# Kernel tuning notes

Hardware: AMD Instinct MI355X
Metric: run time of the kernel (lower is better)

Reference implementation:

```python
import jax, jax.numpy as jnp
import numpy as np

B, R, C, NH = 8, 64, 256, 8
N = R * R            # 4096 tokens
HD = C // NH         # head dim 32
FF = 3               # focusing factor

def dwconv(x, w, b):
    # x: (B, C, H, W); w: (C, 1, kh, kw) depthwise
    y = jax.lax.conv_general_dilated(
        x, w, window_strides=(1, 1), padding='SAME',
        dimension_numbers=('NCHW', 'OIHW', 'NCHW'),
        feature_group_count=x.shape[1])
    return y + b[None, :, None, None]

def setup_inputs() -> dict:
    key = jax.random.key(0)
    ks = jax.random.split(key, 6)
    return {
        'qkv': jax.random.normal(ks[0], (3, B, N, C), jnp.float32),
        'pos_enc': jax.random.normal(ks[1], (1, N, C), jnp.float32) * 0.02,
        'scale': jax.random.normal(ks[2], (1, 1, C), jnp.float32) * 0.02,
        'w_v': jax.random.normal(ks[3], (C, 1, 3, 3), jnp.float32) * 0.1,
        'b_v': jnp.zeros((C,), jnp.float32),
        'w_dwc': jax.random.normal(ks[4], (HD, 1, 5, 5), jnp.float32) * 0.1,
        'b_dwc': jnp.zeros((HD,), jnp.float32),
    }

def reference(qkv, pos_enc, scale, w_v, b_v, w_dwc, b_dwc):
    q, k, v = qkv[0], qkv[1], qkv[2]          # each (B, N, C)
    # --- LePE: depthwise 3x3 conv on v over full channel dim ---
    v_img = v.transpose(0, 2, 1).reshape(B, C, R, R)
    lepe = dwconv(v_img, w_v, b_v)            # (B, C, R, R)
    lepe = lepe.reshape(B * NH, HD, N).transpose(0, 2, 1)   # (B*h, N, hd)
    v = v_img.reshape(B, C, N).transpose(0, 2, 1)           # (B, N, C)
    # --- focused kernelization ---
    k = k + pos_enc
    sc = jax.nn.softplus(scale)
    q = (jax.nn.relu(q) + 1e-6) / sc
    k = (jax.nn.relu(k) + 1e-6) / sc
    qn = jnp.linalg.norm(q, axis=-1, keepdims=True)
    kn = jnp.linalg.norm(k, axis=-1, keepdims=True)
    q = q ** FF
    k = k ** FF
    q = q / jnp.linalg.norm(q, axis=-1, keepdims=True) * qn
    k = k / jnp.linalg.norm(k, axis=-1, keepdims=True) * kn
    split = lambda x: x.reshape(B, N, NH, HD).transpose(0, 2, 1, 3).reshape(B * NH, N, HD)
    q, k, v = split(q), split(k), split(v)    # (B*h, N, hd)
    # --- linear attention (kv aggregation path: N >> hd) ---
    z = 1.0 / (jnp.einsum('bic,bc->bi', q, k.sum(axis=1)) + 1e-6)
    kv = jnp.einsum('bjc,bjd->bcd', k, v)     # (B*h, hd, hd)
    x = jnp.einsum('bic,bcd,bi->bid', q, kv, z)
    # --- dwc feature mixing on v per head ---
    fm = v.transpose(0, 2, 1).reshape(B * NH, HD, R, R)
    fm = dwconv(fm, w_dwc, b_dwc).reshape(B * NH, HD, N).transpose(0, 2, 1)
    x = x + fm + lepe
    x = x.reshape(B, NH, N, HD).transpose(0, 2, 1, 3).reshape(B, N, C)
    return x
```

## Files before the change

kernel.cpp:

```cpp
#include <hip/hip_runtime.h>
#include <math.h>

#define B_  8
#define R_  64
#define C_  256
#define NH_ 8
#define N_  4096
#define HD_ 32

__device__ __forceinline__ float softplus_rcp(float s) {
    return 1.f / __logf(1.f + __expf(s));
}

__global__ __launch_bounds__(256) void kernelN(
        const float* __restrict__ qkv, const float* __restrict__ pos,
        const float* __restrict__ scale,
        float* __restrict__ qs_arr, float* __restrict__ ks_arr) {
    const int t    = threadIdx.x;
    const int wave = t >> 6, lane = t & 63;
    const int tok  = blockIdx.x * 4 + wave;
    const int n    = tok & (N_ - 1);
    const int c0   = lane * 4;

    const size_t qidx = (size_t)tok * C_ + c0;
    const float4 q4 = *(const float4*)(qkv + qidx);
    const float4 k4 = *(const float4*)(qkv + (size_t)B_ * N_ * C_ + qidx);
    const float4 p4 = *(const float4*)(pos + (size_t)n * C_ + c0);
    const float4 s4 = *(const float4*)(scale + c0);

    float qa[4] = {q4.x, q4.y, q4.z, q4.w};
    float ka[4] = {k4.x, k4.y, k4.z, k4.w};
    float pa[4] = {p4.x, p4.y, p4.z, p4.w};
    float sa[4] = {s4.x, s4.y, s4.z, s4.w};

    float sq2 = 0.f, sq6 = 0.f, sk2 = 0.f, sk6 = 0.f;
    #pragma unroll
    for (int i = 0; i < 4; i++) {
        const float rsc = softplus_rcp(sa[i]);
        const float qv = (fmaxf(qa[i], 0.f) + 1e-6f) * rsc;
        const float kv = (fmaxf(ka[i] + pa[i], 0.f) + 1e-6f) * rsc;
        sq2 += qv * qv;  sk2 += kv * kv;
        const float q3 = qv * qv * qv, k3 = kv * kv * kv;
        sq6 += q3 * q3;  sk6 += k3 * k3;
    }
    #pragma unroll
    for (int m = 1; m < 64; m <<= 1) {
        sq2 += __shfl_xor(sq2, m, 64);
        sq6 += __shfl_xor(sq6, m, 64);
        sk2 += __shfl_xor(sk2, m, 64);
        sk6 += __shfl_xor(sk6, m, 64);
    }
    if (lane == 0) {
        qs_arr[tok] = sqrtf(sq2) * rsqrtf(sq6);
        ks_arr[tok] = sqrtf(sk2) * rsqrtf(sk6);
    }
}

__global__ __launch_bounds__(256) void kernelB2(
        const float* __restrict__ qkv, const float* __restrict__ pos,
        const float* __restrict__ scale, const float* __restrict__ ks_arr,
        float* __restrict__ kv_ws, float* __restrict__ ksum_ws) {
    __shared__ float k_s[128 * HD_];
    __shared__ float v_s[128 * HD_];
    __shared__ float rsc_s[HD_];
    const int t     = threadIdx.x;
    const int bh    = blockIdx.x >> 3;
    const int chunk = blockIdx.x & 7;
    const int b     = bh >> 3, h = bh & 7;
    const int c     = t >> 3, p = t & 7, dbase = p * 4;

    if (t < HD_) rsc_s[t] = softplus_rcp(scale[h * HD_ + t]);
    __syncthreads();

    float a0 = 0.f, a1 = 0.f, a2 = 0.f, a3 = 0.f, ksp = 0.f;
    const size_t kbase = (size_t)B_ * N_ * C_ + (size_t)b * N_ * C_ + h * HD_;
    const size_t vbase = (size_t)2 * B_ * N_ * C_ + (size_t)b * N_ * C_ + h * HD_;
    const int tokbase = b * N_;

    for (int tile = 0; tile < 4; tile++) {
        const int n0 = chunk * 512 + tile * 128;
        #pragma unroll
        for (int i = 0; i < 4; i++) {
            const int j  = (i * 256 + t) * 4;
            const int nl = j >> 5, d = j & 31;
            const float4 kr = *(const float4*)(qkv + kbase + (size_t)(n0 + nl) * C_ + d);
            const float4 pr = *(const float4*)(pos + (size_t)(n0 + nl) * C_ + h * HD_ + d);
            const float ksn = ks_arr[tokbase + n0 + nl];
            float4 o;
            {
                float v0 = (fmaxf(kr.x + pr.x, 0.f) + 1e-6f) * rsc_s[d + 0];
                float v1 = (fmaxf(kr.y + pr.y, 0.f) + 1e-6f) * rsc_s[d + 1];
                float v2 = (fmaxf(kr.z + pr.z, 0.f) + 1e-6f) * rsc_s[d + 2];
                float v3 = (fmaxf(kr.w + pr.w, 0.f) + 1e-6f) * rsc_s[d + 3];
                o.x = v0 * v0 * v0 * ksn;  o.y = v1 * v1 * v1 * ksn;
                o.z = v2 * v2 * v2 * ksn;  o.w = v3 * v3 * v3 * ksn;
            }
            *(float4*)&k_s[j] = o;
            ((float4*)v_s)[i * 256 + t] =
                *(const float4*)(qkv + vbase + (size_t)(n0 + nl) * C_ + d);
        }
        __syncthreads();
        #pragma unroll 4
        for (int nl = 0; nl < 128; nl++) {
            const float  kc = k_s[nl * HD_ + c];
            const float4 vv = *(const float4*)&v_s[nl * HD_ + dbase];
            a0 = fmaf(kc, vv.x, a0);
            a1 = fmaf(kc, vv.y, a1);
            a2 = fmaf(kc, vv.z, a2);
            a3 = fmaf(kc, vv.w, a3);
        }
        #pragma unroll
        for (int i = 0; i < 16; i++)
            ksp += k_s[(p + i * 8) * HD_ + c];
        __syncthreads();
    }
    float* kvdst = kv_ws + (size_t)bh * 1024 + c * HD_ + dbase;
    atomicAdd(kvdst + 0, a0);
    atomicAdd(kvdst + 1, a1);
    atomicAdd(kvdst + 2, a2);
    atomicAdd(kvdst + 3, a3);
    k_s[c * 8 + p] = ksp;
    __syncthreads();
    if (t < 32) {
        float s = 0.f;
        #pragma unroll
        for (int i = 0; i < 8; i++) s += k_s[t * 8 + i];
        atomicAdd(&ksum_ws[bh * HD_ + t], s);
    }
}

__global__ __launch_bounds__(256) void kernelCD2(
        const float* __restrict__ qkv, const float* __restrict__ qs_arr,
        const float* __restrict__ kv_ws, const float* __restrict__ ksum_ws,
        const float* __restrict__ scale,
        const float* __restrict__ w_v,  const float* __restrict__ b_v,
        const float* __restrict__ w_dwc, const float* __restrict__ b_dwc,
        float* __restrict__ out) {
    __shared__ float v_s[20 * 20 * 32];
    __shared__ float kv_s[1024];
    __shared__ float ks_s[32];
    __shared__ float rsc_s[32];
    const int t    = threadIdx.x;
    const int tile = blockIdx.x;
    const int h    = blockIdx.y;
    const int b    = blockIdx.z;
    const int ty0  = (tile >> 2) * 16, tx0 = (tile & 3) * 16;
    const int bh   = b * NH_ + h;

    ((float4*)kv_s)[t] = ((const float4*)(kv_ws + (size_t)bh * 1024))[t];
    if (t < 32) {
        ks_s[t]  = ksum_ws[bh * HD_ + t];
        rsc_s[t] = softplus_rcp(scale[h * HD_ + t]);
    }

    const float* vb = qkv + (size_t)2 * B_ * N_ * C_ + (size_t)b * N_ * C_ + h * HD_;
    #pragma unroll
    for (int i = 0; i < 13; i++) {
        const int idx = i * 256 + t;
        if (idx < 3200) {
            const int pix = idx >> 3, d4 = (idx & 7) * 4;
            const int yy = pix / 20, xx = pix - yy * 20;
            const int gy = ty0 + yy - 2, gx = tx0 + xx - 2;
            float4 val = make_float4(0.f, 0.f, 0.f, 0.f);
            if (gy >= 0 && gy < R_ && gx >= 0 && gx < R_)
                val = *(const float4*)(vb + (size_t)(gy * R_ + gx) * C_ + d4);
            *(float4*)&v_s[pix * 32 + d4] = val;
        }
    }

    const int c  = t & 31, pg = t >> 5;
    float wv[9], wd[25];
    {
        const float* wvp = w_v + (size_t)(h * HD_ + c) * 9;
        const float* wdp = w_dwc + (size_t)c * 25;
        #pragma unroll
        for (int i = 0; i < 9; i++)  wv[i] = wvp[i];
        #pragma unroll
        for (int i = 0; i < 25; i++) wd[i] = wdp[i];
    }
    const float bias = b_v[h * HD_ + c] + b_dwc[c];
    __syncthreads();

    float res[32];
    #pragma unroll
    for (int r2 = 0; r2 < 2; r2++) {
        const int ty = pg * 2 + r2;
        float win[5][5];
        #pragma unroll
        for (int j = 0; j < 5; j++)
            #pragma unroll
            for (int i = 0; i < 5; i++)
                win[j][i] = v_s[((ty + i) * 20 + j) * 32 + c];
        #pragma unroll
        for (int tx = 0; tx < 16; tx++) {
            float a = bias;
            #pragma unroll
            for (int j = 0; j < 5; j++) {
                const int slot = (tx + j) % 5;
                #pragma unroll
                for (int i = 0; i < 5; i++)
                    a = fmaf(wd[i * 5 + j], win[slot][i], a);
            }
            #pragma unroll
            for (int j = 1; j < 4; j++) {
                const int slot = (tx + j) % 5;
                #pragma unroll
                for (int i = 1; i < 4; i++)
                    a = fmaf(wv[(i - 1) * 3 + (j - 1)], win[slot][i], a);
            }
            res[r2 * 16 + tx] = a;
            if (tx < 15) {
                const int slot = tx % 5;
                #pragma unroll
                for (int i = 0; i < 5; i++)
                    win[slot][i] = v_s[((ty + i) * 20 + (tx + 5)) * 32 + c];
            }
        }
    }
    __syncthreads();
    #pragma unroll
    for (int r2 = 0; r2 < 2; r2++)
        #pragma unroll
        for (int tx = 0; tx < 16; tx++)
            v_s[((pg * 2 + r2) * 16 + tx) * 33 + c] = res[r2 * 16 + tx];
    __syncthreads();

    {
        const int tyy = t >> 4, txx = t & 15;
        const int n   = (ty0 + tyy) * R_ + (tx0 + txx);
        const int tok = b * N_ + n;
        float q[32];
        const float4* qsrc = (const float4*)(qkv + (size_t)tok * C_ + h * HD_);
        #pragma unroll
        for (int i = 0; i < 8; i++) ((float4*)q)[i] = qsrc[i];
        const float qs = qs_arr[tok];
        #pragma unroll
        for (int i = 0; i < 32; i++) {
            const float r = (fmaxf(q[i], 0.f) + 1e-6f) * rsc_s[i];
            q[i] = r * r * r * qs;
        }

        float denom = 1e-6f;
        #pragma unroll
        for (int cc = 0; cc < 32; cc++) denom = fmaf(q[cc], ks_s[cc], denom);
        const float z = 1.f / denom;

        float o[32];
        #pragma unroll
        for (int i = 0; i < 32; i++) o[i] = 0.f;
        #pragma unroll
        for (int cc = 0; cc < 32; cc++) {
            const float qc = q[cc];
            #pragma unroll
            for (int d = 0; d < 32; d++)
                o[d] = fmaf(qc, kv_s[cc * 32 + d], o[d]);
        }
        float4* dst = (float4*)(out + (size_t)tok * C_ + h * HD_);
        #pragma unroll
        for (int i = 0; i < 8; i++) {
            float4 v4;
            v4.x = fmaf(o[i*4+0], z, v_s[t * 33 + i*4+0]);
            v4.y = fmaf(o[i*4+1], z, v_s[t * 33 + i*4+1]);
            v4.z = fmaf(o[i*4+2], z, v_s[t * 33 + i*4+2]);
            v4.w = fmaf(o[i*4+3], z, v_s[t * 33 + i*4+3]);
            dst[i] = v4;
        }
    }
}

extern "C" void kernel_launch(void* const* d_in, const int* in_sizes, int n_in,
                              void* d_out, int out_size, void* d_ws, size_t ws_size,
                              hipStream_t stream) {
    const float* qkv   = (const float*)d_in[0];
    const float* pos   = (const float*)d_in[1];
    const float* scale = (const float*)d_in[2];
    const float* w_v   = (const float*)d_in[3];
    const float* b_v   = (const float*)d_in[4];
    const float* w_dwc = (const float*)d_in[5];
    const float* b_dwc = (const float*)d_in[6];
    float* out = (float*)d_out;

    float* qs_arr  = (float*)d_ws;
    float* ks_arr  = qs_arr + (size_t)B_ * N_;
    float* kv_ws   = ks_arr + (size_t)B_ * N_;
    float* ksum_ws = kv_ws + 64 * 1024;

    (void)hipMemsetAsync(kv_ws, 0, (64 * 1024 + 64 * 32) * sizeof(float), stream);
    kernelN<<<dim3(B_ * N_ / 4), 256, 0, stream>>>(qkv, pos, scale, qs_arr, ks_arr);
    kernelB2<<<dim3(512), 256, 0, stream>>>(qkv, pos, scale, ks_arr, kv_ws, ksum_ws);
    kernelCD2<<<dim3(16, NH_, B_), 256, 0, stream>>>(qkv, qs_arr, kv_ws, ksum_ws,
                                                     scale, w_v, b_v, w_dwc, b_dwc, out);
}
```

Before: 222.8 us.

## Store conv tile and result exchange in bf16 LDS; double kv-reduction grid

The fused conv/attention kernel now keeps the v halo tile and the conv results in LDS as bf16 instead of fp32, which roughly halves its LDS footprint and should allow more resident blocks. Conv results are written straight into a separate padded exchange buffer, so the register array and one barrier are gone. The kv-aggregation kernel's grid is doubled, with each block covering half as many tokens. The cost is bf16 rounding on v and on the conv outputs, which lowers accuracy, and twice as many atomic adds into the kv workspace.

```diff
diff --git a/kernel.cpp b/kernel.cpp
--- a/kernel.cpp
+++ b/kernel.cpp
@@ -10,6 +10,14 @@
 
 __device__ __forceinline__ float softplus_rcp(float s) {
     return 1.f / __logf(1.f + __expf(s));
+}
+__device__ __forceinline__ unsigned short f2bf(float f) {
+    unsigned u = __float_as_uint(f);
+    u += 0x7FFFu + ((u >> 16) & 1u);
+    return (unsigned short)(u >> 16);
+}
+__device__ __forceinline__ float bf2f(unsigned short h) {
+    return __uint_as_float(((unsigned)h) << 16);
 }
 
 __global__ __launch_bounds__(256) void kernelN(
@@ -64,8 +72,8 @@
     __shared__ float v_s[128 * HD_];
     __shared__ float rsc_s[HD_];
     const int t     = threadIdx.x;
-    const int bh    = blockIdx.x >> 3;
-    const int chunk = blockIdx.x & 7;
+    const int bh    = blockIdx.x >> 4;
+    const int chunk = blockIdx.x & 15;
     const int b     = bh >> 3, h = bh & 7;
     const int c     = t >> 3, p = t & 7, dbase = p * 4;
 
@@ -77,8 +85,8 @@
     const size_t vbase = (size_t)2 * B_ * N_ * C_ + (size_t)b * N_ * C_ + h * HD_;
     const int tokbase = b * N_;
 
-    for (int tile = 0; tile < 4; tile++) {
-        const int n0 = chunk * 512 + tile * 128;
+    for (int tile = 0; tile < 2; tile++) {
+        const int n0 = chunk * 256 + tile * 128;
         #pragma unroll
         for (int i = 0; i < 4; i++) {
             const int j  = (i * 256 + t) * 4;
@@ -129,14 +137,16 @@
     }
 }
 
-__global__ __launch_bounds__(256) void kernelCD2(
+#define EXP_ 258
+__global__ __launch_bounds__(256) void kernelCD3(
         const float* __restrict__ qkv, const float* __restrict__ qs_arr,
         const float* __restrict__ kv_ws, const float* __restrict__ ksum_ws,
         const float* __restrict__ scale,
         const float* __restrict__ w_v,  const float* __restrict__ b_v,
         const float* __restrict__ w_dwc, const float* __restrict__ b_dwc,
         float* __restrict__ out) {
-    __shared__ float v_s[20 * 20 * 32];
+    __shared__ unsigned short v_s[20 * 20 * 32];
+    __shared__ unsigned short exch[HD_ * EXP_];
     __shared__ float kv_s[1024];
     __shared__ float ks_s[32];
     __shared__ float rsc_s[32];
@@ -164,7 +174,10 @@
             float4 val = make_float4(0.f, 0.f, 0.f, 0.f);
             if (gy >= 0 && gy < R_ && gx >= 0 && gx < R_)
                 val = *(const float4*)(vb + (size_t)(gy * R_ + gx) * C_ + d4);
-            *(float4*)&v_s[pix * 32 + d4] = val;
+            ushort4 hv;
+            hv.x = f2bf(val.x);  hv.y = f2bf(val.y);
+            hv.z = f2bf(val.z);  hv.w = f2bf(val.w);
+            *(ushort4*)&v_s[pix * 32 + d4] = hv;
         }
     }
 
@@ -181,7 +194,6 @@
     const float bias = b_v[h * HD_ + c] + b_dwc[c];
     __syncthreads();
 
-    float res[32];
     #pragma unroll
     for (int r2 = 0; r2 < 2; r2++) {
         const int ty = pg * 2 + r2;
@@ -190,7 +202,7 @@
         for (int j = 0; j < 5; j++)
             #pragma unroll
             for (int i = 0; i < 5; i++)
-                win[j][i] = v_s[((ty + i) * 20 + j) * 32 + c];
+                win[j][i] = bf2f(v_s[((ty + i) * 20 + j) * 32 + c]);
         #pragma unroll
         for (int tx = 0; tx < 16; tx++) {
             float a = bias;
@@ -208,21 +220,15 @@
                 for (int i = 1; i < 4; i++)
                     a = fmaf(wv[(i - 1) * 3 + (j - 1)], win[slot][i], a);
             }
-            res[r2 * 16 + tx] = a;
+            exch[c * EXP_ + (ty * 16 + tx)] = f2bf(a);
             if (tx < 15) {
                 const int slot = tx % 5;
                 #pragma unroll
                 for (int i = 0; i < 5; i++)
-                    win[slot][i] = v_s[((ty + i) * 20 + (tx + 5)) * 32 + c];
-            }
-        }
-    }
-    __syncthreads();
-    #pragma unroll
-    for (int r2 = 0; r2 < 2; r2++)
-        #pragma unroll
-        for (int tx = 0; tx < 16; tx++)
-            v_s[((pg * 2 + r2) * 16 + tx) * 33 + c] = res[r2 * 16 + tx];
+                    win[slot][i] = bf2f(v_s[((ty + i) * 20 + (tx + 5)) * 32 + c]);
+            }
+        }
+    }
     __syncthreads();
 
     {
@@ -259,10 +265,10 @@
         #pragma unroll
         for (int i = 0; i < 8; i++) {
             float4 v4;
-            v4.x = fmaf(o[i*4+0], z, v_s[t * 33 + i*4+0]);
-            v4.y = fmaf(o[i*4+1], z, v_s[t * 33 + i*4+1]);
-            v4.z = fmaf(o[i*4+2], z, v_s[t * 33 + i*4+2]);
-            v4.w = fmaf(o[i*4+3], z, v_s[t * 33 + i*4+3]);
+            v4.x = fmaf(o[i*4+0], z, bf2f(exch[(i*4+0) * EXP_ + t]));
+            v4.y = fmaf(o[i*4+1], z, bf2f(exch[(i*4+1) * EXP_ + t]));
+            v4.z = fmaf(o[i*4+2], z, bf2f(exch[(i*4+2) * EXP_ + t]));
+            v4.w = fmaf(o[i*4+3], z, bf2f(exch[(i*4+3) * EXP_ + t]));
             dst[i] = v4;
         }
     }
@@ -287,7 +293,7 @@
 
     (void)hipMemsetAsync(kv_ws, 0, (64 * 1024 + 64 * 32) * sizeof(float), stream);
     kernelN<<<dim3(B_ * N_ / 4), 256, 0, stream>>>(qkv, pos, scale, qs_arr, ks_arr);
-    kernelB2<<<dim3(512), 256, 0, stream>>>(qkv, pos, scale, ks_arr, kv_ws, ksum_ws);
-    kernelCD2<<<dim3(16, NH_, B_), 256, 0, stream>>>(qkv, qs_arr, kv_ws, ksum_ws,
+    kernelB2<<<dim3(1024), 256, 0, stream>>>(qkv, pos, scale, ks_arr, kv_ws, ksum_ws);
+    kernelCD3<<<dim3(16, NH_, B_), 256, 0, stream>>>(qkv, qs_arr, kv_ws, ksum_ws,
                                                      scale, w_v, b_v, w_dwc, b_dwc, out);
 }
```

Result: no change. 225.5 us (+1.2%).

## Fuse norm computation kernel into KV aggregation kernel

Applied to the files above, without the earlier changes.

Merges the per-token norm kernel into the KV-aggregation kernel. Each block now processes 64 tokens of one batch across all 8 heads, computing q/k norms in-register via 16-lane shuffles. It then forms the per-head KV outer product with a 32-wide per-thread accumulator. This avoids one launch, a second read of k and pos from global memory, and the ks_arr round trip. In exchange it adds many more atomics (32 per thread across 512 blocks) and higher register pressure from acc[32].

```diff
diff --git a/kernel.cpp b/kernel.cpp
--- a/kernel.cpp
+++ b/kernel.cpp
@@ -7,126 +7,111 @@
 #define NH_ 8
 #define N_  4096
 #define HD_ 32
+#define TT_ 16
+#define LDP_ 260
 
 __device__ __forceinline__ float softplus_rcp(float s) {
     return 1.f / __logf(1.f + __expf(s));
 }
 
-__global__ __launch_bounds__(256) void kernelN(
+__global__ __launch_bounds__(256) void kernelNB(
         const float* __restrict__ qkv, const float* __restrict__ pos,
         const float* __restrict__ scale,
-        float* __restrict__ qs_arr, float* __restrict__ ks_arr) {
-    const int t    = threadIdx.x;
-    const int wave = t >> 6, lane = t & 63;
-    const int tok  = blockIdx.x * 4 + wave;
-    const int n    = tok & (N_ - 1);
-    const int c0   = lane * 4;
-
-    const size_t qidx = (size_t)tok * C_ + c0;
-    const float4 q4 = *(const float4*)(qkv + qidx);
-    const float4 k4 = *(const float4*)(qkv + (size_t)B_ * N_ * C_ + qidx);
-    const float4 p4 = *(const float4*)(pos + (size_t)n * C_ + c0);
-    const float4 s4 = *(const float4*)(scale + c0);
-
-    float qa[4] = {q4.x, q4.y, q4.z, q4.w};
-    float ka[4] = {k4.x, k4.y, k4.z, k4.w};
-    float pa[4] = {p4.x, p4.y, p4.z, p4.w};
-    float sa[4] = {s4.x, s4.y, s4.z, s4.w};
-
-    float sq2 = 0.f, sq6 = 0.f, sk2 = 0.f, sk6 = 0.f;
-    #pragma unroll
-    for (int i = 0; i < 4; i++) {
-        const float rsc = softplus_rcp(sa[i]);
-        const float qv = (fmaxf(qa[i], 0.f) + 1e-6f) * rsc;
-        const float kv = (fmaxf(ka[i] + pa[i], 0.f) + 1e-6f) * rsc;
-        sq2 += qv * qv;  sk2 += kv * kv;
-        const float q3 = qv * qv * qv, k3 = kv * kv * kv;
-        sq6 += q3 * q3;  sk6 += k3 * k3;
-    }
-    #pragma unroll
-    for (int m = 1; m < 64; m <<= 1) {
-        sq2 += __shfl_xor(sq2, m, 64);
-        sq6 += __shfl_xor(sq6, m, 64);
-        sk2 += __shfl_xor(sk2, m, 64);
-        sk6 += __shfl_xor(sk6, m, 64);
-    }
-    if (lane == 0) {
-        qs_arr[tok] = sqrtf(sq2) * rsqrtf(sq6);
-        ks_arr[tok] = sqrtf(sk2) * rsqrtf(sk6);
-    }
-}
-
-__global__ __launch_bounds__(256) void kernelB2(
-        const float* __restrict__ qkv, const float* __restrict__ pos,
-        const float* __restrict__ scale, const float* __restrict__ ks_arr,
+        float* __restrict__ qs_arr,
         float* __restrict__ kv_ws, float* __restrict__ ksum_ws) {
-    __shared__ float k_s[128 * HD_];
-    __shared__ float v_s[128 * HD_];
-    __shared__ float rsc_s[HD_];
+    __shared__ float k_s[TT_][LDP_];
+    __shared__ float v_s[TT_][LDP_];
+    __shared__ float rsc_s[C_];
     const int t     = threadIdx.x;
-    const int bh    = blockIdx.x >> 3;
-    const int chunk = blockIdx.x & 7;
-    const int b     = bh >> 3, h = bh & 7;
-    const int c     = t >> 3, p = t & 7, dbase = p * 4;
-
-    if (t < HD_) rsc_s[t] = softplus_rcp(scale[h * HD_ + t]);
-    __syncthreads();
-
-    float a0 = 0.f, a1 = 0.f, a2 = 0.f, a3 = 0.f, ksp = 0.f;
-    const size_t kbase = (size_t)B_ * N_ * C_ + (size_t)b * N_ * C_ + h * HD_;
-    const size_t vbase = (size_t)2 * B_ * N_ * C_ + (size_t)b * N_ * C_ + h * HD_;
-    const int tokbase = b * N_;
+    const int b     = blockIdx.x >> 6;
+    const int chunk = blockIdx.x & 63;
+    const int h  = t >> 5, cc = t & 31;
+    const int tk = t >> 4, sub = t & 15;
+
+    rsc_s[t] = softplus_rcp(scale[t]);
+    __syncthreads();
+
+    float acc[32];
+    #pragma unroll
+    for (int i = 0; i < 32; i++) acc[i] = 0.f;
+    float ksp = 0.f;
+
+    const size_t qbase = (size_t)b * N_ * C_;
+    const size_t kbase = (size_t)(B_ + b) * N_ * C_;
+    const size_t vbase = (size_t)(2 * B_ + b) * N_ * C_;
 
     for (int tile = 0; tile < 4; tile++) {
-        const int n0 = chunk * 512 + tile * 128;
+        const int n0  = chunk * 64 + tile * TT_;
+        const int tok = n0 + tk;
+
+        float kva[16];
+        float sq2 = 0.f, sq6 = 0.f, sk2 = 0.f, sk6 = 0.f;
         #pragma unroll
         for (int i = 0; i < 4; i++) {
-            const int j  = (i * 256 + t) * 4;
-            const int nl = j >> 5, d = j & 31;
-            const float4 kr = *(const float4*)(qkv + kbase + (size_t)(n0 + nl) * C_ + d);
-            const float4 pr = *(const float4*)(pos + (size_t)(n0 + nl) * C_ + h * HD_ + d);
-            const float ksn = ks_arr[tokbase + n0 + nl];
+            const int c0 = (sub + i * 16) * 4;
+            const float4 q4 = *(const float4*)(qkv + qbase + (size_t)tok * C_ + c0);
+            const float4 k4 = *(const float4*)(qkv + kbase + (size_t)tok * C_ + c0);
+            const float4 p4 = *(const float4*)(pos + (size_t)tok * C_ + c0);
+            const float qa[4] = {q4.x, q4.y, q4.z, q4.w};
+            const float ka[4] = {k4.x, k4.y, k4.z, k4.w};
+            const float pa[4] = {p4.x, p4.y, p4.z, p4.w};
+            #pragma unroll
+            for (int j = 0; j < 4; j++) {
+                const float rsc = rsc_s[c0 + j];
+                const float qv = (fmaxf(qa[j], 0.f) + 1e-6f) * rsc;
+                const float kv = (fmaxf(ka[j] + pa[j], 0.f) + 1e-6f) * rsc;
+                sq2 += qv * qv;
+                const float q3 = qv * qv * qv;
+                sq6 += q3 * q3;
+                sk2 += kv * kv;
+                const float k3 = kv * kv * kv;
+                sk6 += k3 * k3;
+                kva[i * 4 + j] = kv;
+            }
+        }
+        #pragma unroll
+        for (int m = 1; m < 16; m <<= 1) {
+            sq2 += __shfl_xor(sq2, m, 64);
+            sq6 += __shfl_xor(sq6, m, 64);
+            sk2 += __shfl_xor(sk2, m, 64);
+            sk6 += __shfl_xor(sk6, m, 64);
+        }
+        const float ksn = sqrtf(sk2) * rsqrtf(sk6);
+        if (sub == 0)
+            qs_arr[b * N_ + tok] = sqrtf(sq2) * rsqrtf(sq6);
+
+        #pragma unroll
+        for (int i = 0; i < 4; i++) {
+            const int c0 = (sub + i * 16) * 4;
             float4 o;
-            {
-                float v0 = (fmaxf(kr.x + pr.x, 0.f) + 1e-6f) * rsc_s[d + 0];
-                float v1 = (fmaxf(kr.y + pr.y, 0.f) + 1e-6f) * rsc_s[d + 1];
-                float v2 = (fmaxf(kr.z + pr.z, 0.f) + 1e-6f) * rsc_s[d + 2];
-                float v3 = (fmaxf(kr.w + pr.w, 0.f) + 1e-6f) * rsc_s[d + 3];
-                o.x = v0 * v0 * v0 * ksn;  o.y = v1 * v1 * v1 * ksn;
-                o.z = v2 * v2 * v2 * ksn;  o.w = v3 * v3 * v3 * ksn;
-            }
-            *(float4*)&k_s[j] = o;
-            ((float4*)v_s)[i * 256 + t] =
-                *(const float4*)(qkv + vbase + (size_t)(n0 + nl) * C_ + d);
+            o.x = kva[i*4+0] * kva[i*4+0] * kva[i*4+0] * ksn;
+            o.y = kva[i*4+1] * kva[i*4+1] * kva[i*4+1] * ksn;
+            o.z = kva[i*4+2] * kva[i*4+2] * kva[i*4+2] * ksn;
+            o.w = kva[i*4+3] * kva[i*4+3] * kva[i*4+3] * ksn;
+            *(float4*)&k_s[tk][c0] = o;
+            *(float4*)&v_s[tk][c0] =
+                *(const float4*)(qkv + vbase + (size_t)tok * C_ + c0);
         }
         __syncthreads();
+
         #pragma unroll 4
-        for (int nl = 0; nl < 128; nl++) {
-            const float  kc = k_s[nl * HD_ + c];
-            const float4 vv = *(const float4*)&v_s[nl * HD_ + dbase];
-            a0 = fmaf(kc, vv.x, a0);
-            a1 = fmaf(kc, vv.y, a1);
-            a2 = fmaf(kc, vv.z, a2);
-            a3 = fmaf(kc, vv.w, a3);
-        }
-        #pragma unroll
-        for (int i = 0; i < 16; i++)
-            ksp += k_s[(p + i * 8) * HD_ + c];
+        for (int nl = 0; nl < TT_; nl++) {
+            const float kc = k_s[nl][h * 32 + cc];
+            ksp += kc;
+            const float* vr = &v_s[nl][h * 32];
+            #pragma unroll
+            for (int d = 0; d < 32; d++)
+                acc[d] = fmaf(kc, vr[d], acc[d]);
+        }
         __syncthreads();
     }
-    float* kvdst = kv_ws + (size_t)bh * 1024 + c * HD_ + dbase;
-    atomicAdd(kvdst + 0, a0);
-    atomicAdd(kvdst + 1, a1);
-    atomicAdd(kvdst + 2, a2);
-    atomicAdd(kvdst + 3, a3);
-    k_s[c * 8 + p] = ksp;
-    __syncthreads();
-    if (t < 32) {
-        float s = 0.f;
-        #pragma unroll
-        for (int i = 0; i < 8; i++) s += k_s[t * 8 + i];
-        atomicAdd(&ksum_ws[bh * HD_ + t], s);
-    }
+
+    const int bh = b * NH_ + h;
+    float* kvdst = kv_ws + (size_t)bh * 1024 + cc * 32;
+    #pragma unroll
+    for (int d = 0; d < 32; d++)
+        atomicAdd(kvdst + d, acc[d]);
+    atomicAdd(&ksum_ws[bh * HD_ + cc], ksp);
 }
 
 __global__ __launch_bounds__(256) void kernelCD2(
@@ -281,13 +266,11 @@
     float* out = (float*)d_out;
 
     float* qs_arr  = (float*)d_ws;
-    float* ks_arr  = qs_arr + (size_t)B_ * N_;
-    float* kv_ws   = ks_arr + (size_t)B_ * N_;
+    float* kv_ws   = qs_arr + (size_t)B_ * N_;
     float* ksum_ws = kv_ws + 64 * 1024;
 
     (void)hipMemsetAsync(kv_ws, 0, (64 * 1024 + 64 * 32) * sizeof(float), stream);
-    kernelN<<<dim3(B_ * N_ / 4), 256, 0, stream>>>(qkv, pos, scale, qs_arr, ks_arr);
-    kernelB2<<<dim3(512), 256, 0, stream>>>(qkv, pos, scale, ks_arr, kv_ws, ksum_ws);
+    kernelNB<<<dim3(512), 256, 0, stream>>>(qkv, pos, scale, qs_arr, kv_ws, ksum_ws);
     kernelCD2<<<dim3(16, NH_, B_), 256, 0, stream>>>(qkv, qs_arr, kv_ws, ksum_ws,
                                                      scale, w_v, b_v, w_dwc, b_dwc, out);
 }
```

Measured after the change: 417.9 us. +87.6%, slower.
